# Performance work log

Measured on AMD Instinct MI355X. Metric: run time of the kernel, lower is better.

## Reference

```python
import jax, jax.numpy as jnp
import numpy as np

B, N, M = 8, 2048, 2048
DQ = DK = DV = H = O = 1024

def setup_inputs() -> dict:
    key = jax.random.key(0)
    ks = jax.random.split(key, 10)
    input_query = jax.random.normal(ks[0], (B, N, DQ), dtype=jnp.float32)
    input_key = jax.random.normal(ks[1], (B, M, DK), dtype=jnp.float32)
    input_value = jax.random.normal(ks[2], (B, M, DV), dtype=jnp.float32)
    seq_lens = jax.random.randint(ks[3], (B,), 1, M + 1)
    seq_lens = seq_lens.at[0].set(M)  # original asserts max(seq_lens) == M
    s = 1.0 / np.sqrt(DQ)
    Wq = jax.random.normal(ks[4], (DQ, H), dtype=jnp.float32) * s
    bq = jnp.zeros((H,), dtype=jnp.float32)
    Wk = jax.random.normal(ks[5], (DK, H), dtype=jnp.float32) * s
    bk = jnp.zeros((H,), dtype=jnp.float32)
    Wv = jax.random.normal(ks[6], (DV, O), dtype=jnp.float32) * s
    bv = jnp.zeros((O,), dtype=jnp.float32)
    return {"input_query": input_query, "input_key": input_key, "input_value": input_value,
            "seq_lens": seq_lens, "Wq": Wq, "bq": bq, "Wk": Wk, "bk": bk, "Wv": Wv, "bv": bv}


def reference(input_query, input_key, input_value, seq_lens, Wq, bq, Wk, bk, Wv, bv):
    hidden_dim = Wq.shape[1]
    lq = input_query @ Wq + bq          # (B, N, H)
    lk = input_key @ Wk + bk            # (B, M, H)
    lv = input_value @ Wv + bv          # (B, M, O)
    scores = jnp.einsum('bnh,bmh->bnm', lq, lk) / jnp.sqrt(jnp.float32(hidden_dim))
    # additive mask: 0 for valid positions, finfo.min for padded (as in original)
    valid = (jnp.arange(scores.shape[-1]) < seq_lens[:, None])[:, None, :]  # (B,1,M)
    add_mask = jnp.where(valid, 0.0, jnp.finfo(scores.dtype).min)
    scores = scores + add_mask
    probs = jax.nn.softmax(scores, axis=-1)
    out = jnp.einsum('bnm,bmo->bno', probs, lv)  # dropout is identity in eval
    return out
```

## Files before the change

### kernel.cpp

```cpp
#include <hip/hip_runtime.h>
#include <hip/hip_bf16.h>

typedef unsigned short u16;
typedef __attribute__((ext_vector_type(8))) short bfrag;
typedef __attribute__((ext_vector_type(4))) float f32x4;
typedef __attribute__((ext_vector_type(8))) unsigned short us8;
typedef __attribute__((ext_vector_type(4))) unsigned short us4;

__device__ __forceinline__ u16 f2bf(float f) {
  union { float f; unsigned int u; } x; x.f = f;
  unsigned int r = x.u + 0x7fffu + ((x.u >> 16) & 1u);
  return (u16)(r >> 16);
}
__device__ __forceinline__ float bf2f(u16 u) {
  union { unsigned int u; float f; } x; x.u = ((unsigned int)u) << 16;
  return x.f;
}

__device__ __forceinline__ void gld16(const void* g, void* l) {
  __builtin_amdgcn_global_load_lds((const __attribute__((address_space(1))) void*)g,
                                   (__attribute__((address_space(3))) void*)l, 16, 0, 0);
}

__global__ __launch_bounds__(256) void transpose_w(const float* __restrict__ W0,
                                                   const float* __restrict__ W1,
                                                   const float* __restrict__ W2,
                                                   u16* __restrict__ T0,
                                                   u16* __restrict__ T1,
                                                   u16* __restrict__ T2) {
  const float* W = (blockIdx.z == 0) ? W0 : ((blockIdx.z == 1) ? W1 : W2);
  u16* T = (blockIdx.z == 0) ? T0 : ((blockIdx.z == 1) ? T1 : T2);
  __shared__ u16 tile[64][72];
  const int t = threadIdx.x;
  const int rr = t >> 4;
  const int cc = (t & 15) * 4;
  const int kbase = blockIdx.y * 64, nbase = blockIdx.x * 64;
#pragma unroll
  for (int j = 0; j < 4; ++j) {
    int kl = rr + j * 16;
    float4 v = *(const float4*)(W + (size_t)(kbase + kl) * 1024 + nbase + cc);
    tile[kl][cc + 0] = f2bf(v.x);
    tile[kl][cc + 1] = f2bf(v.y);
    tile[kl][cc + 2] = f2bf(v.z);
    tile[kl][cc + 3] = f2bf(v.w);
  }
  __syncthreads();
#pragma unroll
  for (int j = 0; j < 4; ++j) {
    int nl = rr + j * 16;
    us4 o;
    o[0] = tile[cc + 0][nl];
    o[1] = tile[cc + 1][nl];
    o[2] = tile[cc + 2][nl];
    o[3] = tile[cc + 3][nl];
    *(us4*)(T + (size_t)(nbase + nl) * 1024 + kbase + cc) = o;
  }
}

__global__ __launch_bounds__(256) void cvt_bf16(const float* __restrict__ src,
                                                u16* __restrict__ dst, int n8) {
  int i = blockIdx.x * blockDim.x + threadIdx.x;
  const int stride = gridDim.x * blockDim.x;
  for (; i < n8; i += stride) {
    const float4* p = (const float4*)(src + (size_t)i * 8);
    float4 v0 = p[0], v1 = p[1];
    us8 o;
    o[0] = f2bf(v0.x); o[1] = f2bf(v0.y); o[2] = f2bf(v0.z); o[3] = f2bf(v0.w);
    o[4] = f2bf(v1.x); o[5] = f2bf(v1.y); o[6] = f2bf(v1.z); o[7] = f2bf(v1.w);
    *(us8*)(dst + (size_t)i * 8) = o;
  }
}

template <int OUT, int MAP>
__global__ __launch_bounds__(512, 2) void gemm256(const u16* __restrict__ gA,
                                                  const u16* __restrict__ gB,
                                                  const float* __restrict__ bias,
                                                  void* __restrict__ outp,
                                                  int K, int ldc,
                                                  size_t aStride, size_t bStride,
                                                  size_t cStride,
                                                  const int* __restrict__ seq) {
  __shared__ u16 lds[65536];
  const int tid = threadIdx.x;

  int bx, by, bz;
  if constexpr (MAP == 0) {
    const int id = blockIdx.x + gridDim.x * blockIdx.y;
    bx = (id >> 3) & 3; by = (id & 7) + 8 * (id >> 5); bz = 0;
  } else if constexpr (MAP == 1) {
    const int id = blockIdx.x;
    const int j = (id >> 3) & 15;
    const int S = (id & 7) + 8 * (id >> 7);
    bz = S >> 2;
    const int s4 = S & 3;
    by = (s4 >> 1) * 4 + (j >> 2);
    bx = (s4 & 1) * 4 + (j & 3);
  } else {
    const int id = blockIdx.x;
    const int j = (id >> 3) & 15;
    const int S = (id & 7) + 8 * (id >> 7);
    bz = S >> 1;
    by = (S & 1) * 4 + (j >> 2);
    bx = j & 3;
  }

  const u16* A = gA + (size_t)bz * aStride;
  const u16* B = gB + (size_t)bz * bStride;
  const int brow = by * 256, bcol = bx * 256;

  const int NT = K >> 6;
  int NTe = NT;
  if constexpr (OUT == 1) {
    if (bcol >= seq[bz]) return;
  }
  if constexpr (OUT == 3) {
    const int len = seq[bz];
    const int nt2 = (len + 63) >> 6;
    NTe = nt2 < NT ? nt2 : NT;
  }

  const int wv = tid >> 6, l = tid & 63;
  const int wm = wv >> 2, wn = wv & 3;
  const int fr = l & 15, fq = l >> 4;
  const int g0 = (fq ^ (fr & 7)) * 8;
  const int g1 = ((4 + fq) ^ (fr & 7)) * 8;

  const int srow = tid >> 3;
  const int sg = (tid & 7) ^ (srow & 7);
  const u16* aS = A + (size_t)(brow + srow) * K + sg * 8;
  const u16* bS = B + (size_t)(bcol + srow) * K + sg * 8;
  u16* const dA = lds + wv * 512;
  u16* const dB = lds + 32768 + wv * 512;

  f32x4 acc[8][4] = {};

  auto stA = [&](int tile, int c, int buf) {
    gld16(aS + (size_t)tile * 64 + (size_t)c * 64 * K, dA + buf * 16384 + c * 4096);
  };
  auto stB = [&](int tile, int c, int buf) {
    gld16(bS + (size_t)tile * 64 + (size_t)c * 64 * K, dB + buf * 16384 + c * 4096);
  };

#pragma unroll
  for (int c = 0; c < 4; ++c) stA(0, c, 0);
#pragma unroll
  for (int c = 0; c < 4; ++c) stB(0, c, 0);
  if (NTe > 1) {
    stA(1, 0, 1); stA(1, 2, 1);
    stB(1, 0, 1); stB(1, 1, 1); stB(1, 2, 1); stB(1, 3, 1);
  }

  for (int t = 0; t < NTe; ++t) {
    const int cur = t & 1;
    const u16* At = lds + cur * 16384;
    const u16* Bt = lds + 32768 + cur * 16384;

    if (t + 1 < NTe) asm volatile("s_waitcnt vmcnt(6)" ::: "memory");
    else             asm volatile("s_waitcnt vmcnt(0)" ::: "memory");
    __builtin_amdgcn_s_barrier();

    bfrag a[4][2], b[2][2][2];

#pragma unroll
    for (int m = 0; m < 4; ++m) {
      const u16* p = At + (wm * 128 + m * 16 + fr) * 64;
      a[m][0] = *(const bfrag*)(p + g0);
      a[m][1] = *(const bfrag*)(p + g1);
    }
#pragma unroll
    for (int n = 0; n < 2; ++n) {
      const u16* p = Bt + (wn * 64 + n * 16 + fr) * 64;
      b[0][n][0] = *(const bfrag*)(p + g0);
      b[0][n][1] = *(const bfrag*)(p + g1);
    }
    if (t + 1 < NTe) { stA(t + 1, 1, cur ^ 1); stA(t + 1, 3, cur ^ 1); }
    __builtin_amdgcn_s_barrier();
    asm volatile("s_waitcnt lgkmcnt(0)" ::: "memory");
    __builtin_amdgcn_sched_barrier(0);
    __builtin_amdgcn_s_setprio(1);
#pragma unroll
    for (int n = 0; n < 2; ++n)
#pragma unroll
      for (int m = 0; m < 4; ++m) {
        acc[m][n] = __builtin_amdgcn_mfma_f32_16x16x32_bf16(a[m][0], b[0][n][0], acc[m][n], 0, 0, 0);
        acc[m][n] = __builtin_amdgcn_mfma_f32_16x16x32_bf16(a[m][1], b[0][n][1], acc[m][n], 0, 0, 0);
      }
    __builtin_amdgcn_s_setprio(0);
    __builtin_amdgcn_s_barrier();

#pragma unroll
    for (int n = 0; n < 2; ++n) {
      const u16* p = Bt + (wn * 64 + 32 + n * 16 + fr) * 64;
      b[1][n][0] = *(const bfrag*)(p + g0);
      b[1][n][1] = *(const bfrag*)(p + g1);
    }
    if (t + 2 < NTe) { stA(t + 2, 0, cur); stA(t + 2, 2, cur); }
    __builtin_amdgcn_s_barrier();
    asm volatile("s_waitcnt lgkmcnt(0)" ::: "memory");
    __builtin_amdgcn_sched_barrier(0);
    __builtin_amdgcn_s_setprio(1);
#pragma unroll
    for (int n = 0; n < 2; ++n)
#pragma unroll
      for (int m = 0; m < 4; ++m) {
        acc[m][2 + n] = __builtin_amdgcn_mfma_f32_16x16x32_bf16(a[m][0], b[1][n][0], acc[m][2 + n], 0, 0, 0);
        acc[m][2 + n] = __builtin_amdgcn_mfma_f32_16x16x32_bf16(a[m][1], b[1][n][1], acc[m][2 + n], 0, 0, 0);
      }
    __builtin_amdgcn_s_setprio(0);
    __builtin_amdgcn_s_barrier();

#pragma unroll
    for (int m = 0; m < 4; ++m) {
      const u16* p = At + (wm * 128 + 64 + m * 16 + fr) * 64;
      a[m][0] = *(const bfrag*)(p + g0);
      a[m][1] = *(const bfrag*)(p + g1);
    }
    if (t + 2 < NTe) { stB(t + 2, 0, cur); stB(t + 2, 1, cur); }
    __builtin_amdgcn_s_barrier();
    asm volatile("s_waitcnt lgkmcnt(0)" ::: "memory");
    __builtin_amdgcn_sched_barrier(0);
    __builtin_amdgcn_s_setprio(1);
#pragma unroll
    for (int n = 0; n < 2; ++n)
#pragma unroll
      for (int m = 0; m < 4; ++m) {
        acc[4 + m][n] = __builtin_amdgcn_mfma_f32_16x16x32_bf16(a[m][0], b[0][n][0], acc[4 + m][n], 0, 0, 0);
        acc[4 + m][n] = __builtin_amdgcn_mfma_f32_16x16x32_bf16(a[m][1], b[0][n][1], acc[4 + m][n], 0, 0, 0);
      }
    __builtin_amdgcn_s_setprio(0);
    __builtin_amdgcn_s_barrier();

    if (t + 2 < NTe) { stB(t + 2, 2, cur); stB(t + 2, 3, cur); }
    __builtin_amdgcn_s_setprio(1);
#pragma unroll
    for (int n = 0; n < 2; ++n)
#pragma unroll
      for (int m = 0; m < 4; ++m) {
        acc[4 + m][2 + n] = __builtin_amdgcn_mfma_f32_16x16x32_bf16(a[m][0], b[1][n][0], acc[4 + m][2 + n], 0, 0, 0);
        acc[4 + m][2 + n] = __builtin_amdgcn_mfma_f32_16x16x32_bf16(a[m][1], b[1][n][1], acc[4 + m][2 + n], 0, 0, 0);
      }
    __builtin_amdgcn_s_setprio(0);
    __builtin_amdgcn_s_barrier();
  }

#pragma unroll
  for (int mg = 0; mg < 8; ++mg) {
    const int r0 = brow + wm * 128 + mg * 16 + fq * 4;
#pragma unroll
    for (int n = 0; n < 4; ++n) {
      const int c = bcol + wn * 64 + n * 16 + fr;
      f32x4 vv = acc[mg][n];
      if constexpr (OUT == 0) {
        float bb = bias[c];
        u16* C = (u16*)outp;
#pragma unroll
        for (int j = 0; j < 4; ++j) C[(size_t)(r0 + j) * ldc + c] = f2bf(vv[j] + bb);
      } else if constexpr (OUT == 1) {
        u16* C = (u16*)outp + (size_t)bz * cStride;
#pragma unroll
        for (int j = 0; j < 4; ++j) C[(size_t)(r0 + j) * ldc + c] = f2bf(vv[j] * 0.03125f);
      } else if constexpr (OUT == 2) {
        float bb = bias[c];
        const int bz2 = r0 >> 11, mm = r0 & 2047;
        us4 o;
#pragma unroll
        for (int j = 0; j < 4; ++j) o[j] = f2bf(vv[j] + bb);
        *(us4*)((u16*)outp + ((size_t)bz2 * 1024 + c) * 2048 + mm) = o;
      } else {
        float* C = (float*)outp + (size_t)bz * cStride;
#pragma unroll
        for (int j = 0; j < 4; ++j) C[(size_t)(r0 + j) * ldc + c] = vv[j];
      }
    }
  }
}

__global__ __launch_bounds__(256) void softmax_mask(u16* __restrict__ probs,
                                                    const int* __restrict__ seq) {
  const int bid = blockIdx.x;
  const int b = bid >> 11, n = bid & 2047;
  const int len = seq[b];
  const int len64 = (len + 63) & ~63;
  u16* row = probs + ((size_t)b * 2048 + n) * 2048;
  const int t = threadIdx.x;
  const int w = t >> 6, l = t & 63;

  us8 sv = {};
  if (t * 8 < len) sv = *(const us8*)(row + t * 8);
  float vals[8];
  float vmax = -1e30f;
#pragma unroll
  for (int e = 0; e < 8; ++e) {
    int m = t * 8 + e;
    float x = bf2f(sv[e]);
    vals[e] = (m < len) ? x : -1e30f;
    vmax = fmaxf(vmax, vals[e]);
  }
#pragma unroll
  for (int o = 32; o > 0; o >>= 1) vmax = fmaxf(vmax, __shfl_xor(vmax, o, 64));
  __shared__ float sm[4], ss[4];
  if (l == 0) sm[w] = vmax;
  __syncthreads();
  vmax = fmaxf(fmaxf(sm[0], sm[1]), fmaxf(sm[2], sm[3]));

  float ev[8];
  float sum = 0.f;
#pragma unroll
  for (int e = 0; e < 8; ++e) {
    int m = t * 8 + e;
    float p = (m < len) ? __expf(vals[e] - vmax) : 0.f;
    ev[e] = p;
    sum += p;
  }
#pragma unroll
  for (int o = 32; o > 0; o >>= 1) sum += __shfl_xor(sum, o, 64);
  if (l == 0) ss[w] = sum;
  __syncthreads();
  sum = ss[0] + ss[1] + ss[2] + ss[3];
  float inv = 1.f / sum;
  if (t * 8 < len64) {
    us8 ov;
#pragma unroll
    for (int e = 0; e < 8; ++e) ov[e] = f2bf(ev[e] * inv);
    *(us8*)(row + t * 8) = ov;
  }
}

extern "C" void kernel_launch(void* const* d_in, const int* in_sizes, int n_in,
                              void* d_out, int out_size, void* d_ws, size_t ws_size,
                              hipStream_t stream) {
  const float* q   = (const float*)d_in[0];
  const float* k   = (const float*)d_in[1];
  const float* v   = (const float*)d_in[2];
  const int*   seq = (const int*)d_in[3];
  const float* Wq  = (const float*)d_in[4];
  const float* bq  = (const float*)d_in[5];
  const float* Wk  = (const float*)d_in[6];
  const float* bk  = (const float*)d_in[7];
  const float* Wv  = (const float*)d_in[8];
  const float* bv  = (const float*)d_in[9];
  float* out = (float*)d_out;

  u16* ws = (u16*)d_ws;
  u16* wtq = ws;
  u16* wtk = wtq + (size_t)1024 * 1024;
  u16* wtv = wtk + (size_t)1024 * 1024;
  u16* lq  = wtv + (size_t)1024 * 1024;
  u16* lk  = lq + (size_t)16384 * 1024;
  u16* lvt = lk + (size_t)16384 * 1024;
  u16* probs = lvt + (size_t)16384 * 1024;
  u16* cbuf = probs;

  const size_t S21 = (size_t)2048 * 1024;
  const size_t S22 = (size_t)2048 * 2048;

  transpose_w<<<dim3(16, 16, 3), 256, 0, stream>>>(Wq, Wk, Wv, wtq, wtk, wtv);

  cvt_bf16<<<dim3(2048), 256, 0, stream>>>(q, cbuf, 2097152);
  gemm256<0, 0><<<dim3(4, 64), 512, 0, stream>>>(cbuf, wtq, bq, lq, 1024, 1024, 0, 0, 0, nullptr);
  cvt_bf16<<<dim3(2048), 256, 0, stream>>>(k, cbuf, 2097152);
  gemm256<0, 0><<<dim3(4, 64), 512, 0, stream>>>(cbuf, wtk, bk, lk, 1024, 1024, 0, 0, 0, nullptr);
  cvt_bf16<<<dim3(2048), 256, 0, stream>>>(v, cbuf, 2097152);
  gemm256<2, 0><<<dim3(4, 64), 512, 0, stream>>>(cbuf, wtv, bv, lvt, 1024, 1024, 0, 0, 0, nullptr);

  gemm256<1, 1><<<dim3(512), 512, 0, stream>>>(lq, lk, nullptr, probs, 1024, 2048,
                                               S21, S21, S22, seq);
  softmax_mask<<<dim3(16384), 256, 0, stream>>>(probs, seq);
  gemm256<3, 2><<<dim3(256), 512, 0, stream>>>(probs, lvt, nullptr, out, 2048, 1024,
                                               S22, S21, S21, seq);
}
```

Before: 326.9 us.

## Use persistent atomic work-queue scheduling for masked attention GEMMs

The QK^T and PV GEMMs become persistent kernels with 256 workgroups. Each workgroup pulls tile indices from a global atomic counter, which is zeroed by a memset each launch. Tiles masked out by seq_lens are skipped or shortened, so the goal is to balance the uneven per-batch work across CUs instead of leaving idle or early-exiting blocks in a fixed grid. The change adds atomic and sync overhead per tile. It also changes the tile order, since the old XCD-aware id swizzle (id&7 grouping) is dropped for the persistent kernels, which may hurt L2 locality.

```diff
diff --git a/kernel.cpp b/kernel.cpp
--- a/kernel.cpp
+++ b/kernel.cpp
@@ -71,54 +71,14 @@
   }
 }
 
-template <int OUT, int MAP>
-__global__ __launch_bounds__(512, 2) void gemm256(const u16* __restrict__ gA,
-                                                  const u16* __restrict__ gB,
-                                                  const float* __restrict__ bias,
-                                                  void* __restrict__ outp,
-                                                  int K, int ldc,
-                                                  size_t aStride, size_t bStride,
-                                                  size_t cStride,
-                                                  const int* __restrict__ seq) {
-  __shared__ u16 lds[65536];
-  const int tid = threadIdx.x;
-
-  int bx, by, bz;
-  if constexpr (MAP == 0) {
-    const int id = blockIdx.x + gridDim.x * blockIdx.y;
-    bx = (id >> 3) & 3; by = (id & 7) + 8 * (id >> 5); bz = 0;
-  } else if constexpr (MAP == 1) {
-    const int id = blockIdx.x;
-    const int j = (id >> 3) & 15;
-    const int S = (id & 7) + 8 * (id >> 7);
-    bz = S >> 2;
-    const int s4 = S & 3;
-    by = (s4 >> 1) * 4 + (j >> 2);
-    bx = (s4 & 1) * 4 + (j & 3);
-  } else {
-    const int id = blockIdx.x;
-    const int j = (id >> 3) & 15;
-    const int S = (id & 7) + 8 * (id >> 7);
-    bz = S >> 1;
-    by = (S & 1) * 4 + (j >> 2);
-    bx = j & 3;
-  }
-
-  const u16* A = gA + (size_t)bz * aStride;
-  const u16* B = gB + (size_t)bz * bStride;
-  const int brow = by * 256, bcol = bx * 256;
-
-  const int NT = K >> 6;
-  int NTe = NT;
-  if constexpr (OUT == 1) {
-    if (bcol >= seq[bz]) return;
-  }
-  if constexpr (OUT == 3) {
-    const int len = seq[bz];
-    const int nt2 = (len + 63) >> 6;
-    NTe = nt2 < NT ? nt2 : NT;
-  }
-
+template <int OUT>
+__device__ __forceinline__ void gemm256_tile(const u16* __restrict__ A,
+                                             const u16* __restrict__ B,
+                                             const float* __restrict__ bias,
+                                             void* __restrict__ outp,
+                                             int K, int ldc, size_t cStride,
+                                             int brow, int bcol, int bz, int NTe,
+                                             u16* __restrict__ lds, int tid) {
   const int wv = tid >> 6, l = tid & 63;
   const int wm = wv >> 2, wn = wv & 3;
   const int fr = l & 15, fq = l >> 4;
@@ -272,6 +232,71 @@
         for (int j = 0; j < 4; ++j) C[(size_t)(r0 + j) * ldc + c] = vv[j];
       }
     }
+  }
+}
+
+template <int OUT>
+__global__ __launch_bounds__(512, 2) void gemm256s(const u16* __restrict__ gA,
+                                                   const u16* __restrict__ gB,
+                                                   const float* __restrict__ bias,
+                                                   void* __restrict__ outp,
+                                                   int K, int ldc) {
+  __shared__ u16 lds[65536];
+  const int id = blockIdx.x + gridDim.x * blockIdx.y;
+  const int bx = (id >> 3) & 3, by = (id & 7) + 8 * (id >> 5);
+  gemm256_tile<OUT>(gA, gB, bias, outp, K, ldc, 0,
+                    by * 256, bx * 256, 0, K >> 6, lds, threadIdx.x);
+}
+
+template <int OUT>
+__global__ __launch_bounds__(512, 2) void gemm256p(const u16* __restrict__ gA,
+                                                   const u16* __restrict__ gB,
+                                                   void* __restrict__ outp,
+                                                   int K, int ldc,
+                                                   size_t aStride, size_t bStride,
+                                                   size_t cStride,
+                                                   const int* __restrict__ seq,
+                                                   int* __restrict__ counter,
+                                                   int nItems) {
+  __shared__ u16 lds[65536];
+  __shared__ int s_item;
+  const int tid = threadIdx.x;
+  const int NT = K >> 6;
+
+  for (;;) {
+    __syncthreads();
+    if (tid == 0) s_item = atomicAdd(counter, 1);
+    __syncthreads();
+    const int i = s_item;
+    if (i >= nItems) break;
+
+    int bx, by, bz;
+    const int j = i & 15;
+    if constexpr (OUT == 1) {
+      const int S = i >> 4;
+      bz = S >> 2;
+      const int s4 = S & 3;
+      by = (s4 >> 1) * 4 + (j >> 2);
+      bx = (s4 & 1) * 4 + (j & 3);
+    } else {
+      const int S = i >> 4;
+      bz = S >> 1;
+      by = (S & 1) * 4 + (j >> 2);
+      bx = j & 3;
+    }
+
+    int NTe = NT;
+    if constexpr (OUT == 1) {
+      if (bx * 256 >= seq[bz]) continue;
+    }
+    if constexpr (OUT == 3) {
+      const int nt2 = (seq[bz] + 63) >> 6;
+      NTe = nt2 < NT ? nt2 : NT;
+    }
+
+    gemm256_tile<OUT>(gA + (size_t)bz * aStride, gB + (size_t)bz * bStride,
+                      nullptr, outp, K, ldc, cStride,
+                      by * 256, bx * 256, bz, NTe, lds, tid);
   }
 }
 
@@ -342,7 +367,9 @@
   float* out = (float*)d_out;
 
   u16* ws = (u16*)d_ws;
-  u16* wtq = ws;
+  int* counters = (int*)ws;
+  u16* base = ws + 64;
+  u16* wtq = base;
   u16* wtk = wtq + (size_t)1024 * 1024;
   u16* wtv = wtk + (size_t)1024 * 1024;
   u16* lq  = wtv + (size_t)1024 * 1024;
@@ -354,18 +381,19 @@
   const size_t S21 = (size_t)2048 * 1024;
   const size_t S22 = (size_t)2048 * 2048;
 
+  hipMemsetAsync(counters, 0, 128, stream);
   transpose_w<<<dim3(16, 16, 3), 256, 0, stream>>>(Wq, Wk, Wv, wtq, wtk, wtv);
 
   cvt_bf16<<<dim3(2048), 256, 0, stream>>>(q, cbuf, 2097152);
-  gemm256<0, 0><<<dim3(4, 64), 512, 0, stream>>>(cbuf, wtq, bq, lq, 1024, 1024, 0, 0, 0, nullptr);
+  gemm256s<0><<<dim3(4, 64), 512, 0, stream>>>(cbuf, wtq, bq, lq, 1024, 1024);
   cvt_bf16<<<dim3(2048), 256, 0, stream>>>(k, cbuf, 2097152);
-  gemm256<0, 0><<<dim3(4, 64), 512, 0, stream>>>(cbuf, wtk, bk, lk, 1024, 1024, 0, 0, 0, nullptr);
+  gemm256s<0><<<dim3(4, 64), 512, 0, stream>>>(cbuf, wtk, bk, lk, 1024, 1024);
   cvt_bf16<<<dim3(2048), 256, 0, stream>>>(v, cbuf, 2097152);
-  gemm256<2, 0><<<dim3(4, 64), 512, 0, stream>>>(cbuf, wtv, bv, lvt, 1024, 1024, 0, 0, 0, nullptr);
-
-  gemm256<1, 1><<<dim3(512), 512, 0, stream>>>(lq, lk, nullptr, probs, 1024, 2048,
-                                               S21, S21, S22, seq);
+  gemm256s<2><<<dim3(4, 64), 512, 0, stream>>>(cbuf, wtv, bv, lvt, 1024, 1024);
+
+  gemm256p<1><<<dim3(256), 512, 0, stream>>>(lq, lk, probs, 1024, 2048,
+                                             S21, S21, S22, seq, counters + 0, 512);
   softmax_mask<<<dim3(16384), 256, 0, stream>>>(probs, seq);
-  gemm256<3, 2><<<dim3(256), 512, 0, stream>>>(probs, lvt, nullptr, out, 2048, 1024,
-                                               S22, S21, S21, seq);
-}
+  gemm256p<3><<<dim3(256), 512, 0, stream>>>(probs, lvt, out, 2048, 1024,
+                                             S22, S21, S21, seq, counters + 1, 256);
+}
```

Measured after the change: 332.8 us. No clear change (+1.8%).
